# Kernel tuning notes

Hardware: AMD Instinct MI355X
Metric: run time of the kernel (lower is better)

## Reference

```python
import jax, jax.numpy as jnp
import numpy as np

N = 1000          # num splats
H = W = 256       # image size
P = H * W         # num pixels
EPS = 1e-6


def setup_inputs() -> dict:
    key = jax.random.key(0)
    k1, k2, k3, k4, k5 = jax.random.split(key, 5)
    ys, xs = jnp.meshgrid(jnp.linspace(-1.0, 1.0, H), jnp.linspace(-1.0, 1.0, W), indexing='ij')
    xy = jnp.stack([xs.ravel(), ys.ravel()], axis=-1).astype(jnp.float32)  # (P, 2) pixel grid
    return {
        'rho': jax.random.normal(k1, (N, 1), dtype=jnp.float32),
        'sigma': jax.random.normal(k2, (N, 2), dtype=jnp.float32),
        'coords': jax.random.normal(k3, (N, 2), dtype=jnp.float32),
        'alpha': jax.random.normal(k4, (N, 1), dtype=jnp.float32),
        'colors': jax.random.normal(k5, (N, 3), dtype=jnp.float32),
        'xy': xy,
    }


def reference(rho, sigma, coords, alpha, colors, xy):
    # --- Splatter.call activations on raw parameters ---
    rho_a = jax.nn.sigmoid(rho)               # (N,1) used as correlation
    sigma_a = jnp.tanh(sigma / 2) + 1e-4      # (N,2)
    coords_a = jnp.tanh(coords) - 0.5         # (N,2)
    colors_a = jax.nn.sigmoid(colors)         # (N,3)
    alpha_a = jax.nn.sigmoid(alpha)           # (N,1)

    # --- generate_2D_gaussian_splatting ---
    sx = sigma_a[:, 0:1, None]                # (N,1,1)
    sy = sigma_a[:, 1:2, None]                # (N,1,1)
    r = rho_a.reshape((N, 1, 1)) + EPS
    cov = jnp.concatenate([
        jnp.concatenate([sx ** 2 + EPS, sy * sx * r], axis=-1),
        jnp.concatenate([sx * sy * r, sy ** 2 + EPS], axis=-1),
    ], axis=-2).astype(jnp.float32)           # (N,2,2)
    inv_cov = jnp.linalg.inv(cov)             # (N,2,2)

    # offsets: pixel coord + splat coord (matches original's additive shift)
    d = xy[None, :, :] + coords_a[:, None, :]          # (N,P,2)
    z = jnp.einsum('npi,nij,npj->np', d, -0.5 * inv_cov, d)  # (N,P)
    logdet = jnp.log(jnp.linalg.det(cov) + EPS)        # (N,)
    kernel = z - jnp.log(2 * jnp.pi) + 0.5 * logdet[:, None]  # (N,P) log-density
    kernel = jnp.exp(kernel - kernel.max(axis=0, keepdims=True))  # per-pixel max over splats

    alpha_k = kernel * alpha_a                         # (N,P), alpha_a (N,1) broadcasts
    denom = alpha_k.sum(axis=0, keepdims=True) + EPS   # (1,P)
    rgb = (kernel[..., None] * colors_a[:, None, :3] / denom[..., None]).sum(axis=0)  # (P,3)
    return rgb
```

## Files before the change

### kernel.cpp

```cpp
#include <hip/hip_runtime.h>
#include <math.h>

#define NN    1000
#define NPAD  1024
#define NTILE 32
#define TPW   8
#define LOG2E 1.4426950408889634f
#define LN2PI 1.8378770664093453f

typedef float        f32x4  __attribute__((ext_vector_type(4)));
typedef _Float16     f16x8  __attribute__((ext_vector_type(8)));
typedef unsigned int u32x4v __attribute__((ext_vector_type(4)));

static __device__ __forceinline__ float sigmoidf_(float v) {
    return 1.0f / (1.0f + expf(-v));
}
static __device__ __forceinline__ float ev2(float p, float t, float kq, float x) {
    float u = fmaf(p, x, t);
    return __builtin_amdgcn_exp2f(fmaf(-u, u, kq));
}
static __device__ __forceinline__ unsigned pk2(float a, float b) {
    return __builtin_bit_cast(unsigned, __builtin_amdgcn_cvt_pkrtz(a, b));
}

__global__ __launch_bounds__(1024, 4) void splat_fused(
    const float* __restrict__ rho, const float* __restrict__ sigma,
    const float* __restrict__ coords, const float* __restrict__ alpha,
    const float* __restrict__ colors, float* __restrict__ out)
{
    __shared__ f32x4  Lp4[NPAD/4], Lt4[NPAD/4], Lk4[NPAD/4];
    __shared__ f32x4  Lkq4[16][NPAD/4];
    __shared__ u32x4v Lbf[NTILE][4][4];
    __shared__ float  pm2[64][16];
    __shared__ float  pmg[16];
    __shared__ f32x4  pc4[16][64];

    const int tid  = threadIdx.x;
    const int wave = tid >> 6, lane = tid & 63;
    const int col  = lane & 15, g = lane >> 4;
    const int nchunk = wave & 3, pxq = wave >> 2;
    const int row  = blockIdx.x;
    const float step = 2.0f / 255.0f;
    const float y  = -1.0f + (float)row * step;
    const float xb = -1.0f + (float)(64*pxq + col) * step;
    const float x0 = xb, x1 = xb + 16.f*step, x2 = xb + 32.f*step, x3 = xb + 48.f*step;

    float* Lp = (float*)Lp4; float* Lt = (float*)Lt4; float* Lk = (float*)Lk4;
    {
        const int n = tid;
        float p, q, r_, u0, v0, K;
        if (n >= NN) { p=q=r_=u0=v0=0.f; K=-1e30f; }
        else {
            float sx = tanhf(sigma[2*n]   * 0.5f) + 1e-4f;
            float sy = tanhf(sigma[2*n+1] * 0.5f) + 1e-4f;
            float ra = sigmoidf_(rho[n]) + 1e-6f;
            float cxx = sx*sx + 1e-6f, cyy = sy*sy + 1e-6f;
            float cxy = sx*sy*ra;
            float det = cxx*cyy - cxy*cxy;
            float invdet = 1.0f / det;
            float hl = 0.5f * LOG2E;
            p  = sqrtf(hl * cyy * invdet);
            q  = (-hl * cxy * invdet) / p;
            r_ = sqrtf(hl / cyy);
            float cx = tanhf(coords[2*n])   - 0.5f;
            float cy = tanhf(coords[2*n+1]) - 0.5f;
            u0 = p*cx + q*cy;
            v0 = r_*cy;
            K  = (0.5f * logf(det + 1e-6f) - LN2PI) * LOG2E;
        }
        float t = fmaf(q, y, u0);
        float v = fmaf(r_, y, v0);
        Lp[tid] = p; Lt[tid] = t; Lk[tid] = fmaf(-v, v, K);
    }
    if (tid < 512) {
        int T = tid >> 4, c = (tid >> 2) & 3, g2 = tid & 3;
        unsigned w[4] = {0u,0u,0u,0u};
        #pragma unroll
        for (int j = 0; j < 8; ++j) {
            int n = T*32 + g2*8 + j;
            float act = 0.f;
            if (n < NN)
                act = sigmoidf_((c == 0) ? alpha[n] : colors[3*n + c - 1]);
            unsigned short us = __builtin_bit_cast(unsigned short, (_Float16)act);
            w[j>>1] |= (unsigned)us << (16*(j&1));
        }
        Lbf[T][c][g2] = (u32x4v){w[0], w[1], w[2], w[3]};
    }
    __syncthreads();

    {
        const int q16 = tid & 15, chunk = tid >> 4;
        const float xlo = -1.0f + (float)(16*q16) * step;
        const float xhi = xlo + 15.f*step;
        const int nb = chunk * 16;
        float mx = -3.0e38f;
        #pragma unroll
        for (int i = 0; i < 16; ++i) {
            float p = Lp[nb+i], t = Lt[nb+i], Kp = Lk[nb+i];
            float ulo = fmaf(p, xlo, t);
            float uhi = fmaf(p, xhi, t);
            float pen = (ulo*uhi > 0.f) ? fminf(ulo*ulo, uhi*uhi) : 0.f;
            mx = fmaxf(mx, Kp - pen);
        }
        pm2[chunk][q16] = mx;
    }
    __syncthreads();
    if (tid < 16) {
        float M = -3.0e38f;
        #pragma unroll
        for (int j = 0; j < 64; ++j) M = fmaxf(M, pm2[j][tid]);
        pmg[tid] = M;
    }
    __syncthreads();
    {
        float Kp = Lk[tid];
        float* Lkq = (float*)Lkq4;
        #pragma unroll
        for (int q = 0; q < 16; ++q)
            Lkq[q*NPAD + tid] = Kp - pmg[q];
    }
    u32x4v BfR[TPW];
    #pragma unroll
    for (int t = 0; t < TPW; ++t)
        BfR[t] = (col < 4) ? Lbf[nchunk*TPW + t][col][g] : (u32x4v){0u,0u,0u,0u};
    __syncthreads();

    const int nbase = nchunk*256 + g*8;
    const int G0 = pxq * 4;

    f32x4 C0 = {0.f,0.f,0.f,0.f}, C1 = {0.f,0.f,0.f,0.f};
    f32x4 C2 = {0.f,0.f,0.f,0.f}, C3 = {0.f,0.f,0.f,0.f};
    for (int t = 0; t < TPW; ++t) {
        int q4 = (nbase + t*32) >> 2;
        f32x4 pa  = Lp4[q4],        pb  = Lp4[q4+1];
        f32x4 ta  = Lt4[q4],        tb  = Lt4[q4+1];
        f32x4 k0a = Lkq4[G0+0][q4], k0b = Lkq4[G0+0][q4+1];
        f32x4 k1a = Lkq4[G0+1][q4], k1b = Lkq4[G0+1][q4+1];
        f32x4 k2a = Lkq4[G0+2][q4], k2b = Lkq4[G0+2][q4+1];
        f32x4 k3a = Lkq4[G0+3][q4], k3b = Lkq4[G0+3][q4+1];
        f16x8 Bf = __builtin_bit_cast(f16x8, BfR[t]);

        u32x4v W;
        W = (u32x4v){ pk2(ev2(pa[0],ta[0],k0a[0],x0), ev2(pa[1],ta[1],k0a[1],x0)),
                      pk2(ev2(pa[2],ta[2],k0a[2],x0), ev2(pa[3],ta[3],k0a[3],x0)),
                      pk2(ev2(pb[0],tb[0],k0b[0],x0), ev2(pb[1],tb[1],k0b[1],x0)),
                      pk2(ev2(pb[2],tb[2],k0b[2],x0), ev2(pb[3],tb[3],k0b[3],x0)) };
        C0 = __builtin_amdgcn_mfma_f32_16x16x32_f16(__builtin_bit_cast(f16x8, W), Bf, C0, 0, 0, 0);
        W = (u32x4v){ pk2(ev2(pa[0],ta[0],k1a[0],x1), ev2(pa[1],ta[1],k1a[1],x1)),
                      pk2(ev2(pa[2],ta[2],k1a[2],x1), ev2(pa[3],ta[3],k1a[3],x1)),
                      pk2(ev2(pb[0],tb[0],k1b[0],x1), ev2(pb[1],tb[1],k1b[1],x1)),
                      pk2(ev2(pb[2],tb[2],k1b[2],x1), ev2(pb[3],tb[3],k1b[3],x1)) };
        C1 = __builtin_amdgcn_mfma_f32_16x16x32_f16(__builtin_bit_cast(f16x8, W), Bf, C1, 0, 0, 0);
        W = (u32x4v){ pk2(ev2(pa[0],ta[0],k2a[0],x2), ev2(pa[1],ta[1],k2a[1],x2)),
                      pk2(ev2(pa[2],ta[2],k2a[2],x2), ev2(pa[3],ta[3],k2a[3],x2)),
                      pk2(ev2(pb[0],tb[0],k2b[0],x2), ev2(pb[1],tb[1],k2b[1],x2)),
                      pk2(ev2(pb[2],tb[2],k2b[2],x2), ev2(pb[3],tb[3],k2b[3],x2)) };
        C2 = __builtin_amdgcn_mfma_f32_16x16x32_f16(__builtin_bit_cast(f16x8, W), Bf, C2, 0, 0, 0);
        W = (u32x4v){ pk2(ev2(pa[0],ta[0],k3a[0],x3), ev2(pa[1],ta[1],k3a[1],x3)),
                      pk2(ev2(pa[2],ta[2],k3a[2],x3), ev2(pa[3],ta[3],k3a[3],x3)),
                      pk2(ev2(pb[0],tb[0],k3b[0],x3), ev2(pb[1],tb[1],k3b[1],x3)),
                      pk2(ev2(pb[2],tb[2],k3b[2],x3), ev2(pb[3],tb[3],k3b[3],x3)) };
        C3 = __builtin_amdgcn_mfma_f32_16x16x32_f16(__builtin_bit_cast(f16x8, W), Bf, C3, 0, 0, 0);
    }

    if (col < 4) {
        float* pcf = (float*)pc4;
        #pragma unroll
        for (int i = 0; i < 4; ++i) {
            int r0 = 4*g + i;
            pcf[(wave*64 + r0     )*4 + col] = C0[i];
            pcf[(wave*64 + r0 + 16)*4 + col] = C1[i];
            pcf[(wave*64 + r0 + 32)*4 + col] = C2[i];
            pcf[(wave*64 + r0 + 48)*4 + col] = C3[i];
        }
    }
    __syncthreads();
    if (tid < 256) {
        int px = tid;
        int pq = px >> 6, l = px & 63;
        f32x4 S = pc4[4*pq+0][l] + pc4[4*pq+1][l] + pc4[4*pq+2][l] + pc4[4*pq+3][l];
        float inv = 1.0f / (S[0] + 1e-6f);
        int o = (row*256 + px) * 3;
        out[o] = S[1]*inv; out[o+1] = S[2]*inv; out[o+2] = S[3]*inv;
    }
}

extern "C" void kernel_launch(void* const* d_in, const int* in_sizes, int n_in,
                              void* d_out, int out_size, void* d_ws, size_t ws_size,
                              hipStream_t stream) {
    const float* rho    = (const float*)d_in[0];
    const float* sigma  = (const float*)d_in[1];
    const float* coords = (const float*)d_in[2];
    const float* alpha  = (const float*)d_in[3];
    const float* colors = (const float*)d_in[4];
    float* out = (float*)d_out;

    splat_fused<<<256, 1024, 0, stream>>>(rho, sigma, coords, alpha, colors, out);
}
```

Baseline: 20.56 us.

## Drop per-pixel max shift from exponent and fold it into epsilon term

The kernel no longer builds the 16-variant max-shifted K table in LDS. The inner loop evaluates exp2 against the raw per-splat log-density. The per-pixel-group max only rescales the epsilon in the final normalisation, which keeps the result mathematically equivalent. This removes a shared-memory fill pass, two barriers and most LDS reads in the MFMA loop. The splat activations also switch to hardware exp2/log2/rcp intrinsics. The risk is precision: without the max shift, fp16-packed kernel values can underflow where every splat is far away, and the fast transcendental approximations are less accurate.

```diff
diff --git a/kernel.cpp b/kernel.cpp
--- a/kernel.cpp
+++ b/kernel.cpp
@@ -6,18 +6,22 @@
 #define NTILE 32
 #define TPW   8
 #define LOG2E 1.4426950408889634f
-#define LN2PI 1.8378770664093453f
+#define LOG2_2PI 2.6514961294723187f
 
 typedef float        f32x4  __attribute__((ext_vector_type(4)));
 typedef _Float16     f16x8  __attribute__((ext_vector_type(8)));
 typedef unsigned int u32x4v __attribute__((ext_vector_type(4)));
 
-static __device__ __forceinline__ float sigmoidf_(float v) {
-    return 1.0f / (1.0f + expf(-v));
+static __device__ __forceinline__ float ex2(float x)  { return __builtin_amdgcn_exp2f(x); }
+static __device__ __forceinline__ float lg2(float x)  { return __builtin_amdgcn_logf(x); }
+static __device__ __forceinline__ float rcp_(float x) { return __builtin_amdgcn_rcpf(x); }
+static __device__ __forceinline__ float fsig(float x) { return rcp_(1.f + ex2(-LOG2E * x)); }
+static __device__ __forceinline__ float ftanh2x(float two_x_log2e) {
+    return 1.f - 2.f * rcp_(ex2(two_x_log2e) + 1.f);
 }
-static __device__ __forceinline__ float ev2(float p, float t, float kq, float x) {
+static __device__ __forceinline__ float ev2(float p, float t, float K, float x) {
     float u = fmaf(p, x, t);
-    return __builtin_amdgcn_exp2f(fmaf(-u, u, kq));
+    return ex2(fmaf(-u, u, K));
 }
 static __device__ __forceinline__ unsigned pk2(float a, float b) {
     return __builtin_bit_cast(unsigned, __builtin_amdgcn_cvt_pkrtz(a, b));
@@ -29,7 +33,6 @@
     const float* __restrict__ colors, float* __restrict__ out)
 {
     __shared__ f32x4  Lp4[NPAD/4], Lt4[NPAD/4], Lk4[NPAD/4];
-    __shared__ f32x4  Lkq4[16][NPAD/4];
     __shared__ u32x4v Lbf[NTILE][4][4];
     __shared__ float  pm2[64][16];
     __shared__ float  pmg[16];
@@ -51,22 +54,22 @@
         float p, q, r_, u0, v0, K;
         if (n >= NN) { p=q=r_=u0=v0=0.f; K=-1e30f; }
         else {
-            float sx = tanhf(sigma[2*n]   * 0.5f) + 1e-4f;
-            float sy = tanhf(sigma[2*n+1] * 0.5f) + 1e-4f;
-            float ra = sigmoidf_(rho[n]) + 1e-6f;
+            float sx = ftanh2x(LOG2E * sigma[2*n])   + 1e-4f;
+            float sy = ftanh2x(LOG2E * sigma[2*n+1]) + 1e-4f;
+            float ra = fsig(rho[n]) + 1e-6f;
             float cxx = sx*sx + 1e-6f, cyy = sy*sy + 1e-6f;
             float cxy = sx*sy*ra;
             float det = cxx*cyy - cxy*cxy;
-            float invdet = 1.0f / det;
+            float invdet = rcp_(det);
             float hl = 0.5f * LOG2E;
             p  = sqrtf(hl * cyy * invdet);
-            q  = (-hl * cxy * invdet) / p;
-            r_ = sqrtf(hl / cyy);
-            float cx = tanhf(coords[2*n])   - 0.5f;
-            float cy = tanhf(coords[2*n+1]) - 0.5f;
+            q  = (-hl * cxy * invdet) * rcp_(p);
+            r_ = sqrtf(hl * rcp_(cyy));
+            float cx = ftanh2x((2.f*LOG2E) * coords[2*n])   - 0.5f;
+            float cy = ftanh2x((2.f*LOG2E) * coords[2*n+1]) - 0.5f;
             u0 = p*cx + q*cy;
             v0 = r_*cy;
-            K  = (0.5f * logf(det + 1e-6f) - LN2PI) * LOG2E;
+            K  = 0.5f * lg2(det + 1e-6f) - LOG2_2PI;
         }
         float t = fmaf(q, y, u0);
         float v = fmaf(r_, y, v0);
@@ -80,13 +83,18 @@
             int n = T*32 + g2*8 + j;
             float act = 0.f;
             if (n < NN)
-                act = sigmoidf_((c == 0) ? alpha[n] : colors[3*n + c - 1]);
+                act = fsig((c == 0) ? alpha[n] : colors[3*n + c - 1]);
             unsigned short us = __builtin_bit_cast(unsigned short, (_Float16)act);
             w[j>>1] |= (unsigned)us << (16*(j&1));
         }
         Lbf[T][c][g2] = (u32x4v){w[0], w[1], w[2], w[3]};
     }
     __syncthreads();
+
+    u32x4v BfR[TPW];
+    #pragma unroll
+    for (int t = 0; t < TPW; ++t)
+        BfR[t] = (col < 4) ? Lbf[nchunk*TPW + t][col][g] : (u32x4v){0u,0u,0u,0u};
 
     {
         const int q16 = tid & 15, chunk = tid >> 4;
@@ -109,57 +117,40 @@
         float M = -3.0e38f;
         #pragma unroll
         for (int j = 0; j < 64; ++j) M = fmaxf(M, pm2[j][tid]);
-        pmg[tid] = M;
+        pmg[tid] = 1e-6f * ex2(M);
     }
-    __syncthreads();
-    {
-        float Kp = Lk[tid];
-        float* Lkq = (float*)Lkq4;
-        #pragma unroll
-        for (int q = 0; q < 16; ++q)
-            Lkq[q*NPAD + tid] = Kp - pmg[q];
-    }
-    u32x4v BfR[TPW];
-    #pragma unroll
-    for (int t = 0; t < TPW; ++t)
-        BfR[t] = (col < 4) ? Lbf[nchunk*TPW + t][col][g] : (u32x4v){0u,0u,0u,0u};
-    __syncthreads();
 
     const int nbase = nchunk*256 + g*8;
-    const int G0 = pxq * 4;
 
     f32x4 C0 = {0.f,0.f,0.f,0.f}, C1 = {0.f,0.f,0.f,0.f};
     f32x4 C2 = {0.f,0.f,0.f,0.f}, C3 = {0.f,0.f,0.f,0.f};
     for (int t = 0; t < TPW; ++t) {
         int q4 = (nbase + t*32) >> 2;
-        f32x4 pa  = Lp4[q4],        pb  = Lp4[q4+1];
-        f32x4 ta  = Lt4[q4],        tb  = Lt4[q4+1];
-        f32x4 k0a = Lkq4[G0+0][q4], k0b = Lkq4[G0+0][q4+1];
-        f32x4 k1a = Lkq4[G0+1][q4], k1b = Lkq4[G0+1][q4+1];
-        f32x4 k2a = Lkq4[G0+2][q4], k2b = Lkq4[G0+2][q4+1];
-        f32x4 k3a = Lkq4[G0+3][q4], k3b = Lkq4[G0+3][q4+1];
+        f32x4 pa = Lp4[q4], pb = Lp4[q4+1];
+        f32x4 ta = Lt4[q4], tb = Lt4[q4+1];
+        f32x4 ka = Lk4[q4], kb = Lk4[q4+1];
         f16x8 Bf = __builtin_bit_cast(f16x8, BfR[t]);
 
         u32x4v W;
-        W = (u32x4v){ pk2(ev2(pa[0],ta[0],k0a[0],x0), ev2(pa[1],ta[1],k0a[1],x0)),
-                      pk2(ev2(pa[2],ta[2],k0a[2],x0), ev2(pa[3],ta[3],k0a[3],x0)),
-                      pk2(ev2(pb[0],tb[0],k0b[0],x0), ev2(pb[1],tb[1],k0b[1],x0)),
-                      pk2(ev2(pb[2],tb[2],k0b[2],x0), ev2(pb[3],tb[3],k0b[3],x0)) };
+        W = (u32x4v){ pk2(ev2(pa[0],ta[0],ka[0],x0), ev2(pa[1],ta[1],ka[1],x0)),
+                      pk2(ev2(pa[2],ta[2],ka[2],x0), ev2(pa[3],ta[3],ka[3],x0)),
+                      pk2(ev2(pb[0],tb[0],kb[0],x0), ev2(pb[1],tb[1],kb[1],x0)),
+                      pk2(ev2(pb[2],tb[2],kb[2],x0), ev2(pb[3],tb[3],kb[3],x0)) };
         C0 = __builtin_amdgcn_mfma_f32_16x16x32_f16(__builtin_bit_cast(f16x8, W), Bf, C0, 0, 0, 0);
-        W = (u32x4v){ pk2(ev2(pa[0],ta[0],k1a[0],x1), ev2(pa[1],ta[1],k1a[1],x1)),
-                      pk2(ev2(pa[2],ta[2],k1a[2],x1), ev2(pa[3],ta[3],k1a[3],x1)),
-                      pk2(ev2(pb[0],tb[0],k1b[0],x1), ev2(pb[1],tb[1],k1b[1],x1)),
-                      pk2(ev2(pb[2],tb[2],k1b[2],x1), ev2(pb[3],tb[3],k1b[3],x1)) };
+        W = (u32x4v){ pk2(ev2(pa[0],ta[0],ka[0],x1), ev2(pa[1],ta[1],ka[1],x1)),
+                      pk2(ev2(pa[2],ta[2],ka[2],x1), ev2(pa[3],ta[3],ka[3],x1)),
+                      pk2(ev2(pb[0],tb[0],kb[0],x1), ev2(pb[1],tb[1],kb[1],x1)),
+                      pk2(ev2(pb[2],tb[2],kb[2],x1), ev2(pb[3],tb[3],kb[3],x1)) };
         C1 = __builtin_amdgcn_mfma_f32_16x16x32_f16(__builtin_bit_cast(f16x8, W), Bf, C1, 0, 0, 0);
-        W = (u32x4v){ pk2(ev2(pa[0],ta[0],k2a[0],x2), ev2(pa[1],ta[1],k2a[1],x2)),
-                      pk2(ev2(pa[2],ta[2],k2a[2],x2), ev2(pa[3],ta[3],k2a[3],x2)),
-                      pk2(ev2(pb[0],tb[0],k2b[0],x2), ev2(pb[1],tb[1],k2b[1],x2)),
-                      pk2(ev2(pb[2],tb[2],k2b[2],x2), ev2(pb[3],tb[3],k2b[3],x2)) };
+        W = (u32x4v){ pk2(ev2(pa[0],ta[0],ka[0],x2), ev2(pa[1],ta[1],ka[1],x2)),
+                      pk2(ev2(pa[2],ta[2],ka[2],x2), ev2(pa[3],ta[3],ka[3],x2)),
+                      pk2(ev2(pb[0],tb[0],kb[0],x2), ev2(pb[1],tb[1],kb[1],x2)),
+                      pk2(ev2(pb[2],tb[2],kb[2],x2), ev2(pb[3],tb[3],kb[3],x2)) };
         C2 = __builtin_amdgcn_mfma_f32_16x16x32_f16(__builtin_bit_cast(f16x8, W), Bf, C2, 0, 0, 0);
-        W = (u32x4v){ pk2(ev2(pa[0],ta[0],k3a[0],x3), ev2(pa[1],ta[1],k3a[1],x3)),
-                      pk2(ev2(pa[2],ta[2],k3a[2],x3), ev2(pa[3],ta[3],k3a[3],x3)),
-                      pk2(ev2(pb[0],tb[0],k3b[0],x3), ev2(pb[1],tb[1],k3b[1],x3)),
-                      pk2(ev2(pb[2],tb[2],k3b[2],x3), ev2(pb[3],tb[3],k3b[3],x3)) };
+        W = (u32x4v){ pk2(ev2(pa[0],ta[0],ka[0],x3), ev2(pa[1],ta[1],ka[1],x3)),
+                      pk2(ev2(pa[2],ta[2],ka[2],x3), ev2(pa[3],ta[3],ka[3],x3)),
+                      pk2(ev2(pb[0],tb[0],kb[0],x3), ev2(pb[1],tb[1],kb[1],x3)),
+                      pk2(ev2(pb[2],tb[2],kb[2],x3), ev2(pb[3],tb[3],kb[3],x3)) };
         C3 = __builtin_amdgcn_mfma_f32_16x16x32_f16(__builtin_bit_cast(f16x8, W), Bf, C3, 0, 0, 0);
     }
 
@@ -179,7 +170,7 @@
         int px = tid;
         int pq = px >> 6, l = px & 63;
         f32x4 S = pc4[4*pq+0][l] + pc4[4*pq+1][l] + pc4[4*pq+2][l] + pc4[4*pq+3][l];
-        float inv = 1.0f / (S[0] + 1e-6f);
+        float inv = 1.0f / (S[0] + pmg[px >> 4]);
         int o = (row*256 + px) * 3;
         out[o] = S[1]*inv; out[o+1] = S[2]*inv; out[o+2] = S[3]*inv;
     }
```

Result: faster. 17.95 us, median of 2 (-12.7%).
